# Optimization experiments

Hardware: AMD Instinct MI355X
Metric: run time of the kernel (lower is better)

Reference implementation:

```python
import jax, jax.numpy as jnp
import numpy as np

B, T, D = 512, 512, 128   # batch, time_step, input_dim (soft-label classes)
EMB = 32                  # embedding_size
UNITS = 32                # rnn_utils
L = 2                     # rnn_layer_num
ND = 2                    # dense_num - 1 hidden denses
NC = 11                   # output classes
EPS = 1e-3                # keras BatchNormalization default epsilon


def _gru_step(h, x_t, W, U, b):
    # Keras GRUCell, reset_after=True, gate order [z, r, h], recurrent_activation=sigmoid, activation=relu
    gi = x_t @ W + b[0]            # (B, 3U) input projection + input bias
    gr = h @ U + b[1]              # (B, 3U) recurrent projection + recurrent bias
    iz, ir, ih = jnp.split(gi, 3, axis=-1)
    rz, rr, rh = jnp.split(gr, 3, axis=-1)
    z = jax.nn.sigmoid(iz + rz)
    r = jax.nn.sigmoid(ir + rr)
    hh = jax.nn.relu(ih + r * rh)
    return z * h + (1.0 - z) * hh


def _run_gru(xs, W, U, b):
    # xs: (S, B, F) -> outputs (S, B, UNITS), zero initial state
    h0 = jnp.zeros((xs.shape[1], U.shape[0]), xs.dtype)
    def step(h, x_t):
        h2 = _gru_step(h, x_t, W, U, b)
        return h2, h2
    _, ys = jax.lax.scan(step, h0, xs)
    return ys


def setup_inputs() -> dict:
    key = jax.random.key(0)
    ks = jax.random.split(key, 12)
    s = 0.1
    return {
        "x": jax.random.normal(ks[0], (B, T, D), jnp.float32),
        "emb": jax.random.normal(ks[1], (D, EMB), jnp.float32) * s,
        "Wl": jax.random.normal(ks[2], (L, EMB, 3 * UNITS), jnp.float32) * s,
        "Ul": jax.random.normal(ks[3], (L, UNITS, 3 * UNITS), jnp.float32) * s,
        "bl": jnp.zeros((L, 2, 3 * UNITS), jnp.float32),
        "Wr": jax.random.normal(ks[4], (L, EMB, 3 * UNITS), jnp.float32) * s,
        "Ur": jax.random.normal(ks[5], (L, UNITS, 3 * UNITS), jnp.float32) * s,
        "br": jnp.zeros((L, 2, 3 * UNITS), jnp.float32),
        "bn_gamma": jnp.ones((L, UNITS), jnp.float32),
        "bn_beta": jnp.zeros((L, UNITS), jnp.float32),
        "Wd": jax.random.normal(ks[6], (ND, UNITS, 32), jnp.float32) * s,
        "bd": jnp.zeros((ND, 32), jnp.float32),
        "dbn_gamma": jnp.ones((ND, 32), jnp.float32),
        "dbn_beta": jnp.zeros((ND, 32), jnp.float32),
        "Wf": jax.random.normal(ks[7], (32, NC), jnp.float32) * s,
        "bf": jnp.zeros((NC,), jnp.float32),
    }


def reference(x, emb, Wl, Ul, bl, Wr, Ur, br, bn_gamma, bn_beta,
              Wd, bd, dbn_gamma, dbn_beta, Wf, bf):
    Bsz = x.shape[0]
    idx = jnp.argmax(x, axis=2)             # (B, T) hard labels
    h = emb[idx]                            # (B, T, EMB)
    ht = jnp.transpose(h, (1, 0, 2))        # (T, B, EMB) time-major
    for i in range(L):
        # left GRU consumes items 1..T-1; outputs_left[0] is None (-> zero)
        left = _run_gru(ht[1:], Wl[i], Ul[i], bl[i])             # (T-1, B, U), time t covers items 1..t
        # right GRU consumes items T-2..0 in reverse; outputs_right at time T-1 is None (-> zero)
        right = _run_gru(ht[:-1][::-1], Wr[i], Ur[i], br[i])     # step k is time T-2-k
        zero = jnp.zeros((1, Bsz, UNITS), ht.dtype)
        merged = (jnp.concatenate([zero, left], axis=0)
                  + jnp.concatenate([right[::-1], zero], axis=0))  # (T, B, U)
        # keras BatchNormalization (training): stats over batch AND time, axis=-1
        m = merged.mean(axis=(0, 1))
        v = merged.var(axis=(0, 1))
        ht = bn_gamma[i] * (merged - m) * jax.lax.rsqrt(v + EPS) + bn_beta[i]
    xd = jnp.transpose(ht, (1, 0, 2))       # (B, T, U)
    out = xd
    for j in range(ND):
        # faithful to source bug: every dense reads the layer-stack output `item`, only the last survives
        o = jax.nn.relu(xd @ Wd[j] + bd[j])                     # (B, T, 32)
        # per-time-step BN (original loops over time): stats over batch dim only
        m = o.mean(axis=0, keepdims=True)
        v = o.var(axis=0, keepdims=True)
        out = dbn_gamma[j] * (o - m) * jax.lax.rsqrt(v + EPS) + dbn_beta[j]
    return jax.nn.softmax(out @ Wf + bf, axis=-1)               # (B, T, 11)
```

## Files before the change

### kernel.cpp

```cpp
#include <hip/hip_runtime.h>


#define Bsz 512
#define Tsz 512

typedef unsigned uintv2 __attribute__((ext_vector_type(2)));
typedef _Float16 half8 __attribute__((ext_vector_type(8)));
typedef float f32x4 __attribute__((ext_vector_type(4)));

union H8 { unsigned u[4]; half8 h; };

__device__ __forceinline__ float sigmoid_f(float x) {
    return __builtin_amdgcn_rcpf(1.0f + __expf(-x));
}

__device__ __forceinline__ uintv2 p16(unsigned a, unsigned b) {
#if __has_builtin(__builtin_amdgcn_permlane16_swap)
    return __builtin_amdgcn_permlane16_swap(a, b, false, false);
#else
    asm("v_permlane16_swap_b32 %0, %1" : "+v"(a), "+v"(b));
    uintv2 r; r.x = a; r.y = b; return r;
#endif
}
__device__ __forceinline__ uintv2 p32(unsigned a, unsigned b) {
#if __has_builtin(__builtin_amdgcn_permlane32_swap)
    return __builtin_amdgcn_permlane32_swap(a, b, false, false);
#else
    asm("v_permlane32_swap_b32 %0, %1" : "+v"(a), "+v"(b));
    uintv2 r; r.x = a; r.y = b; return r;
#endif
}

__device__ __forceinline__ void route4(unsigned P0, unsigned P1, unsigned P2, unsigned P3,
                                       unsigned& W0, unsigned& W1, unsigned& W2, unsigned& W3)
{
    uintv2 m = p32(P0, P2);
    uintv2 a = p16(m.x, m.y);
    uintv2 n = p32(P1, P3);
    uintv2 c = p16(n.x, n.y);
    W0 = a.x; W2 = a.y; W1 = c.x; W3 = c.y;
}

__device__ __forceinline__ unsigned pk16(float a, float b) {
    auto h = __builtin_amdgcn_cvt_pkrtz(a, b);
    return __builtin_bit_cast(unsigned, h);
}

__device__ __forceinline__ H8 make_B(float v0, float v1, float v2, float v3,
                                     float v4, float v5, float v6, float v7)
{
    unsigned P0 = pk16(v0, v1), P1 = pk16(v2, v3);
    unsigned P2 = pk16(v4, v5), P3 = pk16(v6, v7);
    H8 b;
    route4(P0, P1, P2, P3, b.u[0], b.u[1], b.u[2], b.u[3]);
    return b;
}

__device__ __forceinline__ void calib_slots(int lane, int cs[8]) {
    unsigned q = (unsigned)(lane >> 4) & 3u;
    unsigned c0 = 4u * q, c1 = 16u + 4u * q;
    unsigned P0 = c0 | ((c0 + 1u) << 16);
    unsigned P1 = (c0 + 2u) | ((c0 + 3u) << 16);
    unsigned P2 = c1 | ((c1 + 1u) << 16);
    unsigned P3 = (c1 + 2u) | ((c1 + 3u) << 16);
    unsigned W0, W1, W2, W3;
    route4(P0, P1, P2, P3, W0, W1, W2, W3);
    cs[0] = W0 & 0xffff; cs[1] = W0 >> 16;
    cs[2] = W1 & 0xffff; cs[3] = W1 >> 16;
    cs[4] = W2 & 0xffff; cs[5] = W2 >> 16;
    cs[6] = W3 & 0xffff; cs[7] = W3 >> 16;
}

__device__ __forceinline__ H8 load_A(const float* __restrict__ M, const int cs[8], int gcol) {
    H8 a;
#pragma unroll
    for (int e = 0; e < 4; ++e)
        a.u[e] = pk16(M[cs[2 * e] * 96 + gcol], M[cs[2 * e + 1] * 96 + gcol]);
    return a;
}

__device__ __forceinline__ f32x4 mfma16(const H8& a, const H8& b, f32x4 c) {
    return __builtin_amdgcn_mfma_f32_16x16x32_f16(a.h, b.h, c, 0, 0, 0);
}

__device__ __forceinline__ float gate1(float az, float ar, float ah, float ai, float h) {
    float z = sigmoid_f(az);
    float r = sigmoid_f(ar);
    float hh = fmaxf(0.f, fmaf(r, ah, ai));
    return hh + z * (h - hh);
}

__global__ __launch_bounds__(256) void lspd_argmax(const float* __restrict__ x, int* __restrict__ idxT)
{
    int wv = threadIdx.x >> 6, lane = threadIdx.x & 63;
    long p = (long)blockIdx.x * 4 + wv;
    const float* xp = x + p * 128;
    float v0 = xp[lane];      int i0 = lane;
    float v1 = xp[64 + lane]; int i1 = 64 + lane;
    if (v1 > v0) { v0 = v1; i0 = i1; }
#pragma unroll
    for (int d = 1; d < 64; d <<= 1) {
        float ov = __shfl_xor(v0, d, 64);
        int   oi = __shfl_xor(i0, d, 64);
        if (ov > v0 || (ov == v0 && oi < i0)) { v0 = ov; i0 = oi; }
    }
    if (lane == 0) idxT[p] = i0;
}

__global__ __launch_bounds__(256) void lspd_tab(
    const float* __restrict__ emb, const float* __restrict__ Wl, const float* __restrict__ bl,
    const float* __restrict__ Wr, const float* __restrict__ br,
    float* __restrict__ tabL, float* __restrict__ tabR)
{
    int flat = blockIdx.x * 256 + threadIdx.x;
    int dir = flat / 12288;
    int r = flat % 12288;
    int i = r / 96, g = r % 96;
    const float* W  = dir ? Wr : Wl;
    const float* bb = dir ? br : bl;
    float acc = bb[g];
#pragma unroll
    for (int k = 0; k < 32; ++k) acc = fmaf(emb[i * 32 + k], W[k * 96 + g], acc);
    (dir ? tabR : tabL)[r] = acc;
}

__global__ __launch_bounds__(64)
__attribute__((amdgpu_waves_per_eu(1, 1)))
void lspd_gru0(
    const int* __restrict__ idxT, const float* __restrict__ tabL, const float* __restrict__ tabR,
    const float* __restrict__ Ul, const float* __restrict__ Ur,
    const float* __restrict__ bl, const float* __restrict__ br,
    float* __restrict__ Lout, float* __restrict__ Rout)
{
    int bid = blockIdx.x;
    int dir = bid >> 5;
    int bg  = bid & 31;
    int lane = threadIdx.x;
    int rl = lane & 15;
    int q  = lane >> 4;
    int b  = bg * 16 + rl;
    const float* U    = dir ? Ur : Ul;
    const float* tab  = dir ? tabR : tabL;
    const float* brec = (dir ? br : bl) + 96;
    float* out        = dir ? Rout : Lout;

    int cs[8];
    calib_slots(lane, cs);

    H8 AUz0 = load_A(U, cs, 0  + rl), AUz1 = load_A(U, cs, 16 + rl);
    H8 AUr0 = load_A(U, cs, 32 + rl), AUr1 = load_A(U, cs, 48 + rl);
    H8 AUh0 = load_A(U, cs, 64 + rl), AUh1 = load_A(U, cs, 80 + rl);
    f32x4 BZ0 = *(const f32x4*)(brec + 0  + 4 * q);
    f32x4 BZ1 = *(const f32x4*)(brec + 16 + 4 * q);
    f32x4 BR0 = *(const f32x4*)(brec + 32 + 4 * q);
    f32x4 BR1 = *(const f32x4*)(brec + 48 + 4 * q);
    f32x4 BH0 = *(const f32x4*)(brec + 64 + 4 * q);
    f32x4 BH1 = *(const f32x4*)(brec + 80 + 4 * q);

    const int* idxrow = idxT + (long)b * Tsz;

#define TT0(s) (dir ? (Tsz - 2 - (s)) : (1 + (s)))
    {
        long zb = ((long)(dir ? Tsz - 1 : 0) * Bsz + b) * 32;
        float4 z4 = make_float4(0.f, 0.f, 0.f, 0.f);
        *(float4*)(out + zb + 4 * q) = z4;
        *(float4*)(out + zb + 16 + 4 * q) = z4;
    }
    long ob = ((long)TT0(0) * Bsz + b) * 32;
    long ostride = (long)(dir ? -1 : 1) * Bsz * 32;

    float4 GAz0, GAz1, GAr0, GAr1, GAh0, GAh1;
    float4 GBz0, GBz1, GBr0, GBr1, GBh0, GBh1;
    {
        long ta = (long)idxrow[TT0(0)] * 96;
        GAz0 = *(const float4*)(tab + ta + 0  + 4 * q);
        GAz1 = *(const float4*)(tab + ta + 16 + 4 * q);
        GAr0 = *(const float4*)(tab + ta + 32 + 4 * q);
        GAr1 = *(const float4*)(tab + ta + 48 + 4 * q);
        GAh0 = *(const float4*)(tab + ta + 64 + 4 * q);
        GAh1 = *(const float4*)(tab + ta + 80 + 4 * q);
        long tb = (long)idxrow[TT0(1)] * 96;
        GBz0 = *(const float4*)(tab + tb + 0  + 4 * q);
        GBz1 = *(const float4*)(tab + tb + 16 + 4 * q);
        GBr0 = *(const float4*)(tab + tb + 32 + 4 * q);
        GBr1 = *(const float4*)(tab + tb + 48 + 4 * q);
        GBh0 = *(const float4*)(tab + tb + 64 + 4 * q);
        GBh1 = *(const float4*)(tab + tb + 80 + 4 * q);
    }
    int i0 = idxrow[TT0(2)];
    int i1 = idxrow[TT0(3)];
    int i2 = idxrow[TT0(4)];
    int i3 = idxrow[TT0(5)];

    float h0 = 0.f, h1 = 0.f, h2 = 0.f, h3 = 0.f, h4 = 0.f, h5 = 0.f, h6 = 0.f, h7 = 0.f;

#define STEP0(Gz0, Gz1, Gr0, Gr1, Gh0, Gh1, IREG, SINEXT)                      \
    {                                                                          \
        H8 Bh = make_B(h0, h1, h2, h3, h4, h5, h6, h7);                        \
        f32x4 Cz0 = mfma16(AUz0, Bh, BZ0);                                     \
        f32x4 Cz1 = mfma16(AUz1, Bh, BZ1);                                     \
        f32x4 Cr0 = mfma16(AUr0, Bh, BR0);                                     \
        f32x4 Cr1 = mfma16(AUr1, Bh, BR1);                                     \
        f32x4 Ch0 = mfma16(AUh0, Bh, BH0);                                     \
        f32x4 Ch1 = mfma16(AUh1, Bh, BH1);                                     \
        long tb2 = (long)IREG * 96;                                            \
        float4 nz0 = *(const float4*)(tab + tb2 + 0  + 4 * q);                 \
        float4 nz1 = *(const float4*)(tab + tb2 + 16 + 4 * q);                 \
        float4 nr0 = *(const float4*)(tab + tb2 + 32 + 4 * q);                 \
        float4 nr1 = *(const float4*)(tab + tb2 + 48 + 4 * q);                 \
        float4 nh0 = *(const float4*)(tab + tb2 + 64 + 4 * q);                 \
        float4 nh1 = *(const float4*)(tab + tb2 + 80 + 4 * q);                 \
        int sn = (SINEXT); if (sn > Tsz - 2) sn = Tsz - 2;                     \
        IREG = idxrow[TT0(sn)];                                                \
        h0 = gate1(Cz0.x + Gz0.x, Cr0.x + Gr0.x, Ch0.x, Gh0.x, h0);            \
        h1 = gate1(Cz0.y + Gz0.y, Cr0.y + Gr0.y, Ch0.y, Gh0.y, h1);            \
        h2 = gate1(Cz0.z + Gz0.z, Cr0.z + Gr0.z, Ch0.z, Gh0.z, h2);            \
        h3 = gate1(Cz0.w + Gz0.w, Cr0.w + Gr0.w, Ch0.w, Gh0.w, h3);            \
        h4 = gate1(Cz1.x + Gz1.x, Cr1.x + Gr1.x, Ch1.x, Gh1.x, h4);            \
        h5 = gate1(Cz1.y + Gz1.y, Cr1.y + Gr1.y, Ch1.y, Gh1.y, h5);            \
        h6 = gate1(Cz1.z + Gz1.z, Cr1.z + Gr1.z, Ch1.z, Gh1.z, h6);            \
        h7 = gate1(Cz1.w + Gz1.w, Cr1.w + Gr1.w, Ch1.w, Gh1.w, h7);            \
        *(float4*)(out + ob + 4 * q) = make_float4(h0, h1, h2, h3);            \
        *(float4*)(out + ob + 16 + 4 * q) = make_float4(h4, h5, h6, h7);       \
        ob += ostride;                                                         \
        Gz0 = nz0; Gz1 = nz1; Gr0 = nr0; Gr1 = nr1; Gh0 = nh0; Gh1 = nh1;      \
    }

    for (int sb = 0; sb < 508; sb += 4) {
        STEP0(GAz0, GAz1, GAr0, GAr1, GAh0, GAh1, i0, sb + 6);
        STEP0(GBz0, GBz1, GBr0, GBr1, GBh0, GBh1, i1, sb + 7);
        STEP0(GAz0, GAz1, GAr0, GAr1, GAh0, GAh1, i2, sb + 8);
        STEP0(GBz0, GBz1, GBr0, GBr1, GBh0, GBh1, i3, sb + 9);
    }
    STEP0(GAz0, GAz1, GAr0, GAr1, GAh0, GAh1, i0, 510);
    STEP0(GBz0, GBz1, GBr0, GBr1, GBh0, GBh1, i1, 510);
    STEP0(GAz0, GAz1, GAr0, GAr1, GAh0, GAh1, i2, 510);
#undef STEP0
#undef TT0
}

__global__ __launch_bounds__(256) void lspd_stats(
    const float* __restrict__ A, const float* __restrict__ Bv, float* __restrict__ part)
{
    __shared__ float sS[256], sQ[256];
    int tid = threadIdx.x;
    size_t base = (size_t)blockIdx.x * 65536 + tid;
    float s = 0.f, q = 0.f;
    for (int i = 0; i < 256; ++i) {
        size_t ix = base + (size_t)i * 256;
        float v = A[ix] + Bv[ix];
        s += v; q = fmaf(v, v, q);
    }
    sS[tid] = s; sQ[tid] = q;
    __syncthreads();
    if (tid < 32) {
        float S = 0.f, Q = 0.f;
        for (int j = 0; j < 8; ++j) { S += sS[tid + 32 * j]; Q += sQ[tid + 32 * j]; }
        part[blockIdx.x * 64 + tid] = S;
        part[blockIdx.x * 64 + 32 + tid] = Q;
    }
}

__global__ __launch_bounds__(256) void lspd_fold1(
    const float* __restrict__ part, const float* __restrict__ g0, const float* __restrict__ be0,
    const float* __restrict__ Wl, const float* __restrict__ Wr,
    const float* __restrict__ bl, const float* __restrict__ br,
    float* __restrict__ WpL, float* __restrict__ WpR,
    float* __restrict__ b4L, float* __restrict__ b4R)
{
    __shared__ float sc[32], tc[32];
    int tid = threadIdx.x;
    if (tid < 32) {
        float S = 0.f, Q = 0.f;
        for (int p = 0; p < 128; ++p) { S += part[p * 64 + tid]; Q += part[p * 64 + 32 + tid]; }
        const float invN = 1.0f / 262144.0f;
        float m = S * invN;
        float v = Q * invN - m * m;
        float s = g0[tid] * __builtin_amdgcn_rsqf(v + 1e-3f);
        sc[tid] = s; tc[tid] = be0[tid] - s * m;
    }
    __syncthreads();
    for (int idx = tid; idx < 6144; idx += 256) {
        int dir = idx / 3072, e = idx % 3072, k = e / 96, g = e % 96;
        const float* W1 = (dir ? Wr : Wl) + 3072;
        (dir ? WpR : WpL)[e] = sc[k] * W1[k * 96 + g];
    }
    {
        int idx = tid;
        int dir = idx >> 7, slot = idx & 127, sub = slot >> 5, cc = slot & 31;
        const float* bb = (dir ? br : bl) + 192;
        const float* W1 = (dir ? Wr : Wl) + 3072;
        float r;
        if (sub == 2) {
            r = bb[96 + 64 + cc];
        } else {
            int g = (sub == 3) ? (64 + cc) : (sub * 32 + cc);
            float acc = bb[g];
            for (int k = 0; k < 32; ++k) acc = fmaf(tc[k], W1[k * 96 + g], acc);
            if (sub < 2) acc += bb[96 + g];
            r = acc;
        }
        (dir ? b4R : b4L)[slot] = r;
    }
}

__global__ __launch_bounds__(64)
__attribute__((amdgpu_waves_per_eu(1, 1)))
void lspd_gru1(
    const float* __restrict__ L0, const float* __restrict__ R0,
    const float* __restrict__ WpL, const float* __restrict__ WpR,
    const float* __restrict__ b4L, const float* __restrict__ b4R,
    const float* __restrict__ Ul1, const float* __restrict__ Ur1,
    float* __restrict__ Lout, float* __restrict__ Rout)
{
    int bid = blockIdx.x;
    int dir = bid >> 5;
    int bg  = bid & 31;
    int lane = threadIdx.x;
    int rl = lane & 15;
    int q  = lane >> 4;
    int b  = bg * 16 + rl;
    const float* U  = dir ? Ur1 : Ul1;
    const float* Wp = dir ? WpR : WpL;
    const float* b4 = dir ? b4R : b4L;
    float* out      = dir ? Rout : Lout;

    int cs[8];
    calib_slots(lane, cs);

    H8 AWz0 = load_A(Wp, cs, 0  + rl), AWz1 = load_A(Wp, cs, 16 + rl);
    H8 AWr0 = load_A(Wp, cs, 32 + rl), AWr1 = load_A(Wp, cs, 48 + rl);
    H8 AWh0 = load_A(Wp, cs, 64 + rl), AWh1 = load_A(Wp, cs, 80 + rl);
    H8 AUz0 = load_A(U, cs, 0  + rl),  AUz1 = load_A(U, cs, 16 + rl);
    H8 AUr0 = load_A(U, cs, 32 + rl),  AUr1 = load_A(U, cs, 48 + rl);
    H8 AUh0 = load_A(U, cs, 64 + rl),  AUh1 = load_A(U, cs, 80 + rl);
    f32x4 BZ0 = *(const f32x4*)(b4 + 0   + 4 * q);
    f32x4 BZ1 = *(const f32x4*)(b4 + 16  + 4 * q);
    f32x4 BR0 = *(const f32x4*)(b4 + 32  + 4 * q);
    f32x4 BR1 = *(const f32x4*)(b4 + 48  + 4 * q);
    f32x4 BH0 = *(const f32x4*)(b4 + 64  + 4 * q);
    f32x4 BH1 = *(const f32x4*)(b4 + 80  + 4 * q);
    f32x4 BI0 = *(const f32x4*)(b4 + 96  + 4 * q);
    f32x4 BI1 = *(const f32x4*)(b4 + 112 + 4 * q);

#define XBASE(s) (((long)(dir ? (Tsz - 2 - (s)) : (1 + (s))) * Bsz + b) * 32)
    {
        long zb = ((long)(dir ? Tsz - 1 : 0) * Bsz + b) * 32;
        float4 z4 = make_float4(0.f, 0.f, 0.f, 0.f);
        *(float4*)(out + zb + 4 * q) = z4;
        *(float4*)(out + zb + 16 + 4 * q) = z4;
    }
    long ob = XBASE(0);
    long ostride = (long)(dir ? -1 : 1) * Bsz * 32;

    float4 la0, lb0, ra0, rb0, la1, lb1, ra1, rb1;
    float4 la2, lb2, ra2, rb2, la3, lb3, ra3, rb3;
    {
        long n0 = XBASE(0);
        la0 = *(const float4*)(L0 + n0 + 4 * q); lb0 = *(const float4*)(L0 + n0 + 16 + 4 * q);
        ra0 = *(const float4*)(R0 + n0 + 4 * q); rb0 = *(const float4*)(R0 + n0 + 16 + 4 * q);
        long n1 = XBASE(1);
        la1 = *(const float4*)(L0 + n1 + 4 * q); lb1 = *(const float4*)(L0 + n1 + 16 + 4 * q);
        ra1 = *(const float4*)(R0 + n1 + 4 * q); rb1 = *(const float4*)(R0 + n1 + 16 + 4 * q);
        long n2 = XBASE(2);
        la2 = *(const float4*)(L0 + n2 + 4 * q); lb2 = *(const float4*)(L0 + n2 + 16 + 4 * q);
        ra2 = *(const float4*)(R0 + n2 + 4 * q); rb2 = *(const float4*)(R0 + n2 + 16 + 4 * q);
        long n3 = XBASE(3);
        la3 = *(const float4*)(L0 + n3 + 4 * q); lb3 = *(const float4*)(L0 + n3 + 16 + 4 * q);
        ra3 = *(const float4*)(R0 + n3 + 4 * q); rb3 = *(const float4*)(R0 + n3 + 16 + 4 * q);
    }
    float h0 = 0.f, h1 = 0.f, h2 = 0.f, h3 = 0.f, h4 = 0.f, h5 = 0.f, h6 = 0.f, h7 = 0.f;

#define STEP1(XLA, XLB, XRA, XRB, SNEXT)                                       \
    {                                                                          \
        H8 Bx = make_B(XLA.x + XRA.x, XLA.y + XRA.y, XLA.z + XRA.z,            \
                       XLA.w + XRA.w, XLB.x + XRB.x, XLB.y + XRB.y,            \
                       XLB.z + XRB.z, XLB.w + XRB.w);                          \
        f32x4 Cz0 = mfma16(AWz0, Bx, BZ0);                                     \
        f32x4 Cz1 = mfma16(AWz1, Bx, BZ1);                                     \
        f32x4 Cr0 = mfma16(AWr0, Bx, BR0);                                     \
        f32x4 Cr1 = mfma16(AWr1, Bx, BR1);                                     \
        f32x4 Ci0 = mfma16(AWh0, Bx, BI0);                                     \
        f32x4 Ci1 = mfma16(AWh1, Bx, BI1);                                     \
        int sn = (SNEXT); if (sn > Tsz - 2) sn = Tsz - 2;                      \
        long nb = XBASE(sn);                                                   \
        XLA = *(const float4*)(L0 + nb + 4 * q);                               \
        XLB = *(const float4*)(L0 + nb + 16 + 4 * q);                          \
        XRA = *(const float4*)(R0 + nb + 4 * q);                               \
        XRB = *(const float4*)(R0 + nb + 16 + 4 * q);                          \
        H8 Bh = make_B(h0, h1, h2, h3, h4, h5, h6, h7);                        \
        Cz0 = mfma16(AUz0, Bh, Cz0);                                           \
        Cz1 = mfma16(AUz1, Bh, Cz1);                                           \
        Cr0 = mfma16(AUr0, Bh, Cr0);                                           \
        Cr1 = mfma16(AUr1, Bh, Cr1);                                           \
        f32x4 Ch0 = mfma16(AUh0, Bh, BH0);                                     \
        f32x4 Ch1 = mfma16(AUh1, Bh, BH1);                                     \
        h0 = gate1(Cz0.x, Cr0.x, Ch0.x, Ci0.x, h0);                            \
        h1 = gate1(Cz0.y, Cr0.y, Ch0.y, Ci0.y, h1);                            \
        h2 = gate1(Cz0.z, Cr0.z, Ch0.z, Ci0.z, h2);                            \
        h3 = gate1(Cz0.w, Cr0.w, Ch0.w, Ci0.w, h3);                            \
        h4 = gate1(Cz1.x, Cr1.x, Ch1.x, Ci1.x, h4);                            \
        h5 = gate1(Cz1.y, Cr1.y, Ch1.y, Ci1.y, h5);                            \
        h6 = gate1(Cz1.z, Cr1.z, Ch1.z, Ci1.z, h6);                            \
        h7 = gate1(Cz1.w, Cr1.w, Ch1.w, Ci1.w, h7);                            \
        *(float4*)(out + ob + 4 * q) = make_float4(h0, h1, h2, h3);            \
        *(float4*)(out + ob + 16 + 4 * q) = make_float4(h4, h5, h6, h7);       \
        ob += ostride;                                                         \
    }

    for (int sb = 0; sb < 508; sb += 4) {
        STEP1(la0, lb0, ra0, rb0, sb + 4);
        STEP1(la1, lb1, ra1, rb1, sb + 5);
        STEP1(la2, lb2, ra2, rb2, sb + 6);
        STEP1(la3, lb3, ra3, rb3, sb + 7);
    }
    STEP1(la0, lb0, ra0, rb0, 510);
    STEP1(la1, lb1, ra1, rb1, 510);
    STEP1(la2, lb2, ra2, rb2, 510);
#undef STEP1
#undef XBASE
}

__global__ __launch_bounds__(256) void lspd_fold2(
    const float* __restrict__ part, const float* __restrict__ g1, const float* __restrict__ be1,
    const float* __restrict__ Wd1, const float* __restrict__ bd1,
    float* __restrict__ Wdp, float* __restrict__ bdp)
{
    __shared__ float sc[32], tc[32];
    int tid = threadIdx.x;
    if (tid < 32) {
        float S = 0.f, Q = 0.f;
        for (int p = 0; p < 128; ++p) { S += part[p * 64 + tid]; Q += part[p * 64 + 32 + tid]; }
        const float invN = 1.0f / 262144.0f;
        float m = S * invN;
        float v = Q * invN - m * m;
        float s = g1[tid] * __builtin_amdgcn_rsqf(v + 1e-3f);
        sc[tid] = s; tc[tid] = be1[tid] - s * m;
    }
    __syncthreads();
    for (int idx = tid; idx < 1024; idx += 256) {
        int k = idx >> 5;
        Wdp[idx] = sc[k] * Wd1[idx];
    }
    if (tid < 32) {
        float acc = bd1[tid];
        for (int k = 0; k < 32; ++k) acc = fmaf(tc[k], Wd1[k * 32 + tid], acc);
        bdp[tid] = acc;
    }
}

__global__ __launch_bounds__(512) void lspd_final(
    const float* __restrict__ L1a, const float* __restrict__ R1a,
    const float* __restrict__ Wdp, const float* __restrict__ bdp,
    const float* __restrict__ dg, const float* __restrict__ db,
    const float* __restrict__ Wf, const float* __restrict__ bfv,
    float* __restrict__ outp)
{
    __shared__ alignas(16) float sW[1024];
    __shared__ float sb[32], sWf[352], sbf[16], sS[32], sT[32];
    __shared__ float redS[8][32], redQ[8][32];
    int tid = threadIdx.x, t = blockIdx.x;
    for (int i = tid; i < 1024; i += 512) sW[i] = Wdp[i];
    if (tid < 32)  sb[tid] = bdp[tid];
    if (tid < 352) sWf[tid] = Wf[tid];
    if (tid < 11)  sbf[tid] = bfv[tid];
    __syncthreads();

    size_t base = ((size_t)t * Bsz + tid) * 32;
    float xv[32];
#pragma unroll
    for (int c2 = 0; c2 < 32; c2 += 4) {
        float4 a = *(const float4*)(L1a + base + c2);
        float4 b = *(const float4*)(R1a + base + c2);
        xv[c2 + 0] = a.x + b.x; xv[c2 + 1] = a.y + b.y;
        xv[c2 + 2] = a.z + b.z; xv[c2 + 3] = a.w + b.w;
    }
    float o[32];
#pragma unroll
    for (int g = 0; g < 32; ++g) o[g] = sb[g];
#pragma unroll
    for (int k = 0; k < 32; ++k) {
        float xk = xv[k];
#pragma unroll
        for (int g4 = 0; g4 < 8; ++g4) {
            float4 w = *(const float4*)(sW + k * 32 + g4 * 4);
            o[g4 * 4 + 0] = fmaf(xk, w.x, o[g4 * 4 + 0]);
            o[g4 * 4 + 1] = fmaf(xk, w.y, o[g4 * 4 + 1]);
            o[g4 * 4 + 2] = fmaf(xk, w.z, o[g4 * 4 + 2]);
            o[g4 * 4 + 3] = fmaf(xk, w.w, o[g4 * 4 + 3]);
        }
    }
#pragma unroll
    for (int g = 0; g < 32; ++g) o[g] = fmaxf(o[g], 0.f);

    int wv = tid >> 6, lane = tid & 63;
    for (int g = 0; g < 32; ++g) {
        float s = o[g], q = o[g] * o[g];
        for (int d = 1; d < 64; d <<= 1) {
            s += __shfl_xor(s, d, 64);
            q += __shfl_xor(q, d, 64);
        }
        if (lane == 0) { redS[wv][g] = s; redQ[wv][g] = q; }
    }
    __syncthreads();
    if (tid < 32) {
        float S = 0.f, Q = 0.f;
        for (int w2 = 0; w2 < 8; ++w2) { S += redS[w2][tid]; Q += redQ[w2][tid]; }
        float m = S * (1.0f / 512.0f);
        float v = Q * (1.0f / 512.0f) - m * m;
        float s = dg[tid] * __builtin_amdgcn_rsqf(v + 1e-3f);
        sS[tid] = s; sT[tid] = db[tid] - s * m;
    }
    __syncthreads();

    float lg[11];
#pragma unroll
    for (int n = 0; n < 11; ++n) lg[n] = sbf[n];
#pragma unroll
    for (int g = 0; g < 32; ++g) {
        float no = fmaf(o[g], sS[g], sT[g]);
#pragma unroll
        for (int n = 0; n < 11; ++n) lg[n] = fmaf(no, sWf[g * 11 + n], lg[n]);
    }
    float mx = lg[0];
#pragma unroll
    for (int n = 1; n < 11; ++n) mx = fmaxf(mx, lg[n]);
    float sum = 0.f;
#pragma unroll
    for (int n = 0; n < 11; ++n) { lg[n] = __expf(lg[n] - mx); sum += lg[n]; }
    float inv = __builtin_amdgcn_rcpf(sum);
    float* op = outp + ((size_t)tid * Tsz + t) * 11;
#pragma unroll
    for (int n = 0; n < 11; ++n) op[n] = lg[n] * inv;
}

extern "C" void kernel_launch(void* const* d_in, const int* in_sizes, int n_in,
                              void* d_out, int out_size, void* d_ws, size_t ws_size,
                              hipStream_t stream)
{
    (void)in_sizes; (void)n_in; (void)out_size; (void)ws_size;
    const float* x   = (const float*)d_in[0];
    const float* emb = (const float*)d_in[1];
    const float* Wl  = (const float*)d_in[2];
    const float* Ul  = (const float*)d_in[3];
    const float* bl  = (const float*)d_in[4];
    const float* Wr  = (const float*)d_in[5];
    const float* Ur  = (const float*)d_in[6];
    const float* br  = (const float*)d_in[7];
    const float* bng = (const float*)d_in[8];
    const float* bnb = (const float*)d_in[9];
    const float* Wd  = (const float*)d_in[10];
    const float* bd  = (const float*)d_in[11];
    const float* dg  = (const float*)d_in[12];
    const float* db  = (const float*)d_in[13];
    const float* Wf  = (const float*)d_in[14];
    const float* bf  = (const float*)d_in[15];
    float* out = (float*)d_out;

    float* ws = (float*)d_ws;
    float* L0 = ws;
    float* R0 = L0 + 8388608;
    float* L1 = R0 + 8388608;
    float* R1 = L1 + 8388608;
    float* rest = R1 + 8388608;
    int* idxT   = (int*)rest;
    float* tabL = rest + 262144;
    float* tabR = tabL + 12288;
    float* part1 = tabR + 12288;
    float* part2 = part1 + 8192;
    float* WpL = part2 + 8192;
    float* WpR = WpL + 3072;
    float* b4L = WpR + 3072;
    float* b4R = b4L + 128;
    float* Wdp = b4R + 128;
    float* bdp = Wdp + 1024;

    lspd_argmax<<<65536, 256, 0, stream>>>(x, idxT);
    lspd_tab<<<96, 256, 0, stream>>>(emb, Wl, bl, Wr, br, tabL, tabR);
    lspd_gru0<<<64, 64, 0, stream>>>(idxT, tabL, tabR, Ul, Ur, bl, br, L0, R0);
    lspd_stats<<<128, 256, 0, stream>>>(L0, R0, part1);
    lspd_fold1<<<1, 256, 0, stream>>>(part1, bng, bnb, Wl, Wr, bl, br, WpL, WpR, b4L, b4R);
    lspd_gru1<<<64, 64, 0, stream>>>(L0, R0, WpL, WpR, b4L, b4R, Ul + 3072, Ur + 3072, L1, R1);
    lspd_stats<<<128, 256, 0, stream>>>(L1, R1, part2);
    lspd_fold2<<<1, 256, 0, stream>>>(part2, bng + 32, bnb + 32, Wd + 1024, bd + 32, Wdp, bdp);
    lspd_final<<<512, 512, 0, stream>>>(L1, R1, Wdp, bdp, dg + 32, db + 32, Wf, bf, out);
}
```

Measured before the change: 730.3 us.

## Deepen prefetch in layer-0 GRU and software-pipeline input MFMAs in layer-1

In the layer-0 recurrent kernel, gate-table rows are now prefetched four steps ahead instead of two, and each row is loaded directly into its slot after the gate update rather than through temporaries. In the layer-1 kernel, the input-projection MFMAs for step t+1 are issued during step t, with results double-buffered in two register sets. This takes the input projection off the serial recurrent dependency chain so it can overlap with the recurrent MFMAs and gate math. The cost is higher register pressure, which could lower occupancy or cause spills.

```diff
diff --git a/kernel.cpp b/kernel.cpp
--- a/kernel.cpp
+++ b/kernel.cpp
@@ -169,28 +169,28 @@
     long ob = ((long)TT0(0) * Bsz + b) * 32;
     long ostride = (long)(dir ? -1 : 1) * Bsz * 32;
 
-    float4 GAz0, GAz1, GAr0, GAr1, GAh0, GAh1;
-    float4 GBz0, GBz1, GBr0, GBr1, GBh0, GBh1;
-    {
-        long ta = (long)idxrow[TT0(0)] * 96;
-        GAz0 = *(const float4*)(tab + ta + 0  + 4 * q);
-        GAz1 = *(const float4*)(tab + ta + 16 + 4 * q);
-        GAr0 = *(const float4*)(tab + ta + 32 + 4 * q);
-        GAr1 = *(const float4*)(tab + ta + 48 + 4 * q);
-        GAh0 = *(const float4*)(tab + ta + 64 + 4 * q);
-        GAh1 = *(const float4*)(tab + ta + 80 + 4 * q);
-        long tb = (long)idxrow[TT0(1)] * 96;
-        GBz0 = *(const float4*)(tab + tb + 0  + 4 * q);
-        GBz1 = *(const float4*)(tab + tb + 16 + 4 * q);
-        GBr0 = *(const float4*)(tab + tb + 32 + 4 * q);
-        GBr1 = *(const float4*)(tab + tb + 48 + 4 * q);
-        GBh0 = *(const float4*)(tab + tb + 64 + 4 * q);
-        GBh1 = *(const float4*)(tab + tb + 80 + 4 * q);
-    }
-    int i0 = idxrow[TT0(2)];
-    int i1 = idxrow[TT0(3)];
-    int i2 = idxrow[TT0(4)];
-    int i3 = idxrow[TT0(5)];
+    float4 G0z0, G0z1, G0r0, G0r1, G0h0, G0h1;
+    float4 G1z0, G1z1, G1r0, G1r1, G1h0, G1h1;
+    float4 G2z0, G2z1, G2r0, G2r1, G2h0, G2h1;
+    float4 G3z0, G3z1, G3r0, G3r1, G3h0, G3h1;
+#define GFILL(P, TA)                                                           \
+    {                                                                          \
+        long ta_ = (long)(TA) * 96;                                            \
+        P##z0 = *(const float4*)(tab + ta_ + 0  + 4 * q);                      \
+        P##z1 = *(const float4*)(tab + ta_ + 16 + 4 * q);                      \
+        P##r0 = *(const float4*)(tab + ta_ + 32 + 4 * q);                      \
+        P##r1 = *(const float4*)(tab + ta_ + 48 + 4 * q);                      \
+        P##h0 = *(const float4*)(tab + ta_ + 64 + 4 * q);                      \
+        P##h1 = *(const float4*)(tab + ta_ + 80 + 4 * q);                      \
+    }
+    GFILL(G0, idxrow[TT0(0)]);
+    GFILL(G1, idxrow[TT0(1)]);
+    GFILL(G2, idxrow[TT0(2)]);
+    GFILL(G3, idxrow[TT0(3)]);
+    int i0 = idxrow[TT0(4)];
+    int i1 = idxrow[TT0(5)];
+    int i2 = idxrow[TT0(6)];
+    int i3 = idxrow[TT0(7)];
 
     float h0 = 0.f, h1 = 0.f, h2 = 0.f, h3 = 0.f, h4 = 0.f, h5 = 0.f, h6 = 0.f, h7 = 0.f;
 
@@ -203,15 +203,6 @@
         f32x4 Cr1 = mfma16(AUr1, Bh, BR1);                                     \
         f32x4 Ch0 = mfma16(AUh0, Bh, BH0);                                     \
         f32x4 Ch1 = mfma16(AUh1, Bh, BH1);                                     \
-        long tb2 = (long)IREG * 96;                                            \
-        float4 nz0 = *(const float4*)(tab + tb2 + 0  + 4 * q);                 \
-        float4 nz1 = *(const float4*)(tab + tb2 + 16 + 4 * q);                 \
-        float4 nr0 = *(const float4*)(tab + tb2 + 32 + 4 * q);                 \
-        float4 nr1 = *(const float4*)(tab + tb2 + 48 + 4 * q);                 \
-        float4 nh0 = *(const float4*)(tab + tb2 + 64 + 4 * q);                 \
-        float4 nh1 = *(const float4*)(tab + tb2 + 80 + 4 * q);                 \
-        int sn = (SINEXT); if (sn > Tsz - 2) sn = Tsz - 2;                     \
-        IREG = idxrow[TT0(sn)];                                                \
         h0 = gate1(Cz0.x + Gz0.x, Cr0.x + Gr0.x, Ch0.x, Gh0.x, h0);            \
         h1 = gate1(Cz0.y + Gz0.y, Cr0.y + Gr0.y, Ch0.y, Gh0.y, h1);            \
         h2 = gate1(Cz0.z + Gz0.z, Cr0.z + Gr0.z, Ch0.z, Gh0.z, h2);            \
@@ -223,19 +214,28 @@
         *(float4*)(out + ob + 4 * q) = make_float4(h0, h1, h2, h3);            \
         *(float4*)(out + ob + 16 + 4 * q) = make_float4(h4, h5, h6, h7);       \
         ob += ostride;                                                         \
-        Gz0 = nz0; Gz1 = nz1; Gr0 = nr0; Gr1 = nr1; Gh0 = nh0; Gh1 = nh1;      \
+        long tb2 = (long)IREG * 96;                                            \
+        Gz0 = *(const float4*)(tab + tb2 + 0  + 4 * q);                        \
+        Gz1 = *(const float4*)(tab + tb2 + 16 + 4 * q);                        \
+        Gr0 = *(const float4*)(tab + tb2 + 32 + 4 * q);                        \
+        Gr1 = *(const float4*)(tab + tb2 + 48 + 4 * q);                        \
+        Gh0 = *(const float4*)(tab + tb2 + 64 + 4 * q);                        \
+        Gh1 = *(const float4*)(tab + tb2 + 80 + 4 * q);                        \
+        int sn = (SINEXT); if (sn > Tsz - 2) sn = Tsz - 2;                     \
+        IREG = idxrow[TT0(sn)];                                                \
     }
 
     for (int sb = 0; sb < 508; sb += 4) {
-        STEP0(GAz0, GAz1, GAr0, GAr1, GAh0, GAh1, i0, sb + 6);
-        STEP0(GBz0, GBz1, GBr0, GBr1, GBh0, GBh1, i1, sb + 7);
-        STEP0(GAz0, GAz1, GAr0, GAr1, GAh0, GAh1, i2, sb + 8);
-        STEP0(GBz0, GBz1, GBr0, GBr1, GBh0, GBh1, i3, sb + 9);
-    }
-    STEP0(GAz0, GAz1, GAr0, GAr1, GAh0, GAh1, i0, 510);
-    STEP0(GBz0, GBz1, GBr0, GBr1, GBh0, GBh1, i1, 510);
-    STEP0(GAz0, GAz1, GAr0, GAr1, GAh0, GAh1, i2, 510);
+        STEP0(G0z0, G0z1, G0r0, G0r1, G0h0, G0h1, i0, sb + 8);
+        STEP0(G1z0, G1z1, G1r0, G1r1, G1h0, G1h1, i1, sb + 9);
+        STEP0(G2z0, G2z1, G2r0, G2r1, G2h0, G2h1, i2, sb + 10);
+        STEP0(G3z0, G3z1, G3r0, G3r1, G3h0, G3h1, i3, sb + 11);
+    }
+    STEP0(G0z0, G0z1, G0r0, G0r1, G0h0, G0h1, i0, 510);
+    STEP0(G1z0, G1z1, G1r0, G1r1, G1h0, G1h1, i1, 510);
+    STEP0(G2z0, G2z1, G2r0, G2r1, G2h0, G2h1, i2, 510);
 #undef STEP0
+#undef GFILL
 #undef TT0
 }
 
@@ -353,70 +353,102 @@
     long ob = XBASE(0);
     long ostride = (long)(dir ? -1 : 1) * Bsz * 32;
 
+    f32x4 PAz0, PAz1, PAr0, PAr1, PAi0, PAi1;
+    f32x4 PBz0, PBz1, PBr0, PBr1, PBi0, PBi1;
+    {
+        long n0 = XBASE(0);
+        float4 ta = *(const float4*)(L0 + n0 + 4 * q);
+        float4 tb = *(const float4*)(L0 + n0 + 16 + 4 * q);
+        float4 tc = *(const float4*)(R0 + n0 + 4 * q);
+        float4 td = *(const float4*)(R0 + n0 + 16 + 4 * q);
+        H8 Bx = make_B(ta.x + tc.x, ta.y + tc.y, ta.z + tc.z, ta.w + tc.w,
+                       tb.x + td.x, tb.y + td.y, tb.z + td.z, tb.w + td.w);
+        PAz0 = mfma16(AWz0, Bx, BZ0);
+        PAz1 = mfma16(AWz1, Bx, BZ1);
+        PAr0 = mfma16(AWr0, Bx, BR0);
+        PAr1 = mfma16(AWr1, Bx, BR1);
+        PAi0 = mfma16(AWh0, Bx, BI0);
+        PAi1 = mfma16(AWh1, Bx, BI1);
+    }
     float4 la0, lb0, ra0, rb0, la1, lb1, ra1, rb1;
     float4 la2, lb2, ra2, rb2, la3, lb3, ra3, rb3;
     {
-        long n0 = XBASE(0);
-        la0 = *(const float4*)(L0 + n0 + 4 * q); lb0 = *(const float4*)(L0 + n0 + 16 + 4 * q);
-        ra0 = *(const float4*)(R0 + n0 + 4 * q); rb0 = *(const float4*)(R0 + n0 + 16 + 4 * q);
         long n1 = XBASE(1);
-        la1 = *(const float4*)(L0 + n1 + 4 * q); lb1 = *(const float4*)(L0 + n1 + 16 + 4 * q);
-        ra1 = *(const float4*)(R0 + n1 + 4 * q); rb1 = *(const float4*)(R0 + n1 + 16 + 4 * q);
+        la0 = *(const float4*)(L0 + n1 + 4 * q); lb0 = *(const float4*)(L0 + n1 + 16 + 4 * q);
+        ra0 = *(const float4*)(R0 + n1 + 4 * q); rb0 = *(const float4*)(R0 + n1 + 16 + 4 * q);
         long n2 = XBASE(2);
-        la2 = *(const float4*)(L0 + n2 + 4 * q); lb2 = *(const float4*)(L0 + n2 + 16 + 4 * q);
-        ra2 = *(const float4*)(R0 + n2 + 4 * q); rb2 = *(const float4*)(R0 + n2 + 16 + 4 * q);
+        la1 = *(const float4*)(L0 + n2 + 4 * q); lb1 = *(const float4*)(L0 + n2 + 16 + 4 * q);
+        ra1 = *(const float4*)(R0 + n2 + 4 * q); rb1 = *(const float4*)(R0 + n2 + 16 + 4 * q);
         long n3 = XBASE(3);
-        la3 = *(const float4*)(L0 + n3 + 4 * q); lb3 = *(const float4*)(L0 + n3 + 16 + 4 * q);
-        ra3 = *(const float4*)(R0 + n3 + 4 * q); rb3 = *(const float4*)(R0 + n3 + 16 + 4 * q);
+        la2 = *(const float4*)(L0 + n3 + 4 * q); lb2 = *(const float4*)(L0 + n3 + 16 + 4 * q);
+        ra2 = *(const float4*)(R0 + n3 + 4 * q); rb2 = *(const float4*)(R0 + n3 + 16 + 4 * q);
+        long n4 = XBASE(4);
+        la3 = *(const float4*)(L0 + n4 + 4 * q); lb3 = *(const float4*)(L0 + n4 + 16 + 4 * q);
+        ra3 = *(const float4*)(R0 + n4 + 4 * q); rb3 = *(const float4*)(R0 + n4 + 16 + 4 * q);
     }
     float h0 = 0.f, h1 = 0.f, h2 = 0.f, h3 = 0.f, h4 = 0.f, h5 = 0.f, h6 = 0.f, h7 = 0.f;
 
-#define STEP1(XLA, XLB, XRA, XRB, SNEXT)                                       \
+#define STEP1(XLA, XLB, XRA, XRB, Pz0, Pz1, Pr0, Pr1, Pi0, Pi1,                \
+              Qz0, Qz1, Qr0, Qr1, Qi0, Qi1, SNEXT)                             \
     {                                                                          \
+        H8 Bh = make_B(h0, h1, h2, h3, h4, h5, h6, h7);                        \
+        f32x4 Cz0 = mfma16(AUz0, Bh, Pz0);                                     \
+        f32x4 Cz1 = mfma16(AUz1, Bh, Pz1);                                     \
+        f32x4 Cr0 = mfma16(AUr0, Bh, Pr0);                                     \
+        f32x4 Cr1 = mfma16(AUr1, Bh, Pr1);                                     \
+        f32x4 Ch0 = mfma16(AUh0, Bh, BH0);                                     \
+        f32x4 Ch1 = mfma16(AUh1, Bh, BH1);                                     \
         H8 Bx = make_B(XLA.x + XRA.x, XLA.y + XRA.y, XLA.z + XRA.z,            \
                        XLA.w + XRA.w, XLB.x + XRB.x, XLB.y + XRB.y,            \
                        XLB.z + XRB.z, XLB.w + XRB.w);                          \
-        f32x4 Cz0 = mfma16(AWz0, Bx, BZ0);                                     \
-        f32x4 Cz1 = mfma16(AWz1, Bx, BZ1);                                     \
-        f32x4 Cr0 = mfma16(AWr0, Bx, BR0);                                     \
-        f32x4 Cr1 = mfma16(AWr1, Bx, BR1);                                     \
-        f32x4 Ci0 = mfma16(AWh0, Bx, BI0);                                     \
-        f32x4 Ci1 = mfma16(AWh1, Bx, BI1);                                     \
+        Qz0 = mfma16(AWz0, Bx, BZ0);                                           \
+        Qz1 = mfma16(AWz1, Bx, BZ1);                                           \
+        Qr0 = mfma16(AWr0, Bx, BR0);                                           \
+        Qr1 = mfma16(AWr1, Bx, BR1);                                           \
+        Qi0 = mfma16(AWh0, Bx, BI0);                                           \
+        Qi1 = mfma16(AWh1, Bx, BI1);                                           \
         int sn = (SNEXT); if (sn > Tsz - 2) sn = Tsz - 2;                      \
         long nb = XBASE(sn);                                                   \
         XLA = *(const float4*)(L0 + nb + 4 * q);                               \
         XLB = *(const float4*)(L0 + nb + 16 + 4 * q);                          \
         XRA = *(const float4*)(R0 + nb + 4 * q);                               \
         XRB = *(const float4*)(R0 + nb + 16 + 4 * q);                          \
-        H8 Bh = make_B(h0, h1, h2, h3, h4, h5, h6, h7);                        \
-        Cz0 = mfma16(AUz0, Bh, Cz0);                                           \
-        Cz1 = mfma16(AUz1, Bh, Cz1);                                           \
-        Cr0 = mfma16(AUr0, Bh, Cr0);                                           \
-        Cr1 = mfma16(AUr1, Bh, Cr1);                                           \
-        f32x4 Ch0 = mfma16(AUh0, Bh, BH0);                                     \
-        f32x4 Ch1 = mfma16(AUh1, Bh, BH1);                                     \
-        h0 = gate1(Cz0.x, Cr0.x, Ch0.x, Ci0.x, h0);                            \
-        h1 = gate1(Cz0.y, Cr0.y, Ch0.y, Ci0.y, h1);                            \
-        h2 = gate1(Cz0.z, Cr0.z, Ch0.z, Ci0.z, h2);                            \
-        h3 = gate1(Cz0.w, Cr0.w, Ch0.w, Ci0.w, h3);                            \
-        h4 = gate1(Cz1.x, Cr1.x, Ch1.x, Ci1.x, h4);                            \
-        h5 = gate1(Cz1.y, Cr1.y, Ch1.y, Ci1.y, h5);                            \
-        h6 = gate1(Cz1.z, Cr1.z, Ch1.z, Ci1.z, h6);                            \
-        h7 = gate1(Cz1.w, Cr1.w, Ch1.w, Ci1.w, h7);                            \
+        h0 = gate1(Cz0.x, Cr0.x, Ch0.x, Pi0.x, h0);                            \
+        h1 = gate1(Cz0.y, Cr0.y, Ch0.y, Pi0.y, h1);                            \
+        h2 = gate1(Cz0.z, Cr0.z, Ch0.z, Pi0.z, h2);                            \
+        h3 = gate1(Cz0.w, Cr0.w, Ch0.w, Pi0.w, h3);                            \
+        h4 = gate1(Cz1.x, Cr1.x, Ch1.x, Pi1.x, h4);                            \
+        h5 = gate1(Cz1.y, Cr1.y, Ch1.y, Pi1.y, h5);                            \
+        h6 = gate1(Cz1.z, Cr1.z, Ch1.z, Pi1.z, h6);                            \
+        h7 = gate1(Cz1.w, Cr1.w, Ch1.w, Pi1.w, h7);                            \
         *(float4*)(out + ob + 4 * q) = make_float4(h0, h1, h2, h3);            \
         *(float4*)(out + ob + 16 + 4 * q) = make_float4(h4, h5, h6, h7);       \
         ob += ostride;                                                         \
     }
 
     for (int sb = 0; sb < 508; sb += 4) {
-        STEP1(la0, lb0, ra0, rb0, sb + 4);
-        STEP1(la1, lb1, ra1, rb1, sb + 5);
-        STEP1(la2, lb2, ra2, rb2, sb + 6);
-        STEP1(la3, lb3, ra3, rb3, sb + 7);
-    }
-    STEP1(la0, lb0, ra0, rb0, 510);
-    STEP1(la1, lb1, ra1, rb1, 510);
-    STEP1(la2, lb2, ra2, rb2, 510);
+        STEP1(la0, lb0, ra0, rb0,
+              PAz0, PAz1, PAr0, PAr1, PAi0, PAi1,
+              PBz0, PBz1, PBr0, PBr1, PBi0, PBi1, sb + 5);
+        STEP1(la1, lb1, ra1, rb1,
+              PBz0, PBz1, PBr0, PBr1, PBi0, PBi1,
+              PAz0, PAz1, PAr0, PAr1, PAi0, PAi1, sb + 6);
+        STEP1(la2, lb2, ra2, rb2,
+              PAz0, PAz1, PAr0, PAr1, PAi0, PAi1,
+              PBz0, PBz1, PBr0, PBr1, PBi0, PBi1, sb + 7);
+        STEP1(la3, lb3, ra3, rb3,
+              PBz0, PBz1, PBr0, PBr1, PBi0, PBi1,
+              PAz0, PAz1, PAr0, PAr1, PAi0, PAi1, sb + 8);
+    }
+    STEP1(la0, lb0, ra0, rb0,
+          PAz0, PAz1, PAr0, PAr1, PAi0, PAi1,
+          PBz0, PBz1, PBr0, PBr1, PBi0, PBi1, 510);
+    STEP1(la1, lb1, ra1, rb1,
+          PBz0, PBz1, PBr0, PBr1, PBi0, PBi1,
+          PAz0, PAz1, PAr0, PAr1, PAi0, PAi1, 510);
+    STEP1(la2, lb2, ra2, rb2,
+          PAz0, PAz1, PAr0, PAr1, PAi0, PAi1,
+          PBz0, PBz1, PBr0, PBr1, PBi0, PBi1, 510);
 #undef STEP1
 #undef XBASE
 }
```

Result: no change. 737.5 us (+1.0%).
